# Kernel optimization log

Measured on AMD Instinct MI355X. Metric: run time of the kernel, lower is better.

The kernel has to match this reference:

```python
import jax, jax.numpy as jnp
import numpy as np

N = 50000        # nodes
E = 800000       # edges (before self loops)
F_IN = 128       # input feature dim
HID = 64         # hidden channels per head
HEADS = 4        # heads for layers 1,2 (conv_out has 1 head)
OUT = 40         # num classes
NEG_SLOPE = 0.2  # PyG GATConv default LeakyReLU slope


def gat_layer(x, src, dst, W, att_src, att_dst, b, num_nodes):
    """PyG-style GATConv (concat=True, inference: no dropout).

    x: [N, F_in], W: [F_in, H*C], att_*: [H, C], b: [H*C].
    """
    H, C = att_src.shape
    xw = (x @ W).reshape(num_nodes, H, C)            # [N, H, C]
    a_s = jnp.sum(xw * att_src[None], axis=-1)       # [N, H] per-node src logit
    a_d = jnp.sum(xw * att_dst[None], axis=-1)       # [N, H] per-node dst logit
    e = jax.nn.leaky_relu(a_s[src] + a_d[dst], NEG_SLOPE)  # [E, H]
    # segment softmax over incoming edges of each dst node
    emax = jax.ops.segment_max(e, dst, num_segments=num_nodes)   # [N, H]
    ee = jnp.exp(e - emax[dst])                                  # [E, H]
    denom = jax.ops.segment_sum(ee, dst, num_segments=num_nodes) # [N, H]
    alpha = ee / (denom[dst] + 1e-16)                            # [E, H]
    # scatter-weighted aggregation of source features
    msg = alpha[:, :, None] * xw[src]                            # [E, H, C]
    out = jax.ops.segment_sum(msg, dst, num_segments=num_nodes)  # [N, H, C]
    return out.reshape(num_nodes, H * C) + b


def setup_inputs() -> dict:
    key = jax.random.key(0)
    ks = jax.random.split(key, 12)

    def glorot(k, shape):
        lim = float(np.sqrt(6.0 / (shape[0] + shape[-1])))
        return jax.random.uniform(k, shape, jnp.float32, -lim, lim)

    x = jax.random.normal(ks[0], (N, F_IN), jnp.float32)
    edge_index = jax.random.randint(ks[1], (2, E), 0, N, dtype=jnp.int32)
    inp = {
        "x": x,
        "edge_index": edge_index,
        # layer 1: 128 -> 4 heads x 64
        "W1": glorot(ks[2], (F_IN, HEADS * HID)),
        "a1_src": glorot(ks[3], (HEADS, HID)),
        "a1_dst": glorot(ks[4], (HEADS, HID)),
        "b1": jnp.zeros((HEADS * HID,), jnp.float32),
        # layer 2: 256 -> 4 heads x 64
        "W2": glorot(ks[5], (HEADS * HID, HEADS * HID)),
        "a2_src": glorot(ks[6], (HEADS, HID)),
        "a2_dst": glorot(ks[7], (HEADS, HID)),
        "b2": jnp.zeros((HEADS * HID,), jnp.float32),
        # output layer: 256 -> 1 head x 40
        "W3": glorot(ks[8], (HEADS * HID, OUT)),
        "a3_src": glorot(ks[9], (1, OUT)),
        "a3_dst": glorot(ks[10], (1, OUT)),
        "b3": jnp.zeros((OUT,), jnp.float32),
    }
    return inp


def reference(x, edge_index, W1, a1_src, a1_dst, b1, W2, a2_src, a2_dst, b2,
              W3, a3_src, a3_dst, b3):
    # PyG GATConv adds self loops by default
    loop = jnp.arange(N, dtype=edge_index.dtype)
    src = jnp.concatenate([edge_index[0], loop])
    dst = jnp.concatenate([edge_index[1], loop])

    h = jax.nn.elu(gat_layer(x, src, dst, W1, a1_src, a1_dst, b1, N))
    h = jax.nn.elu(gat_layer(h, src, dst, W2, a2_src, a2_dst, b2, N))
    h = gat_layer(h, src, dst, W3, a3_src, a3_dst, b3, N)
    return jax.nn.log_softmax(h, axis=1)
```

## Files before the change

kernel.cpp:

```cpp
#include <hip/hip_runtime.h>
#include <hip/hip_bf16.h>

#define NN 50000
#define NE 800000

using bf16x8 = __attribute__((ext_vector_type(8))) short;
using f32x4  = __attribute__((ext_vector_type(4))) float;
using f32x2  = __attribute__((ext_vector_type(2))) float;

__device__ __forceinline__ ushort f2bf(float f) {
  uint x = __float_as_uint(f);
  return (ushort)((x + 0x7FFFu + ((x >> 16) & 1u)) >> 16);
}
__device__ __forceinline__ float bf2f(ushort u) {
  return __uint_as_float(((uint)u) << 16);
}
__device__ __forceinline__ float leaky(float x) { return fmaxf(x, 0.2f * x); }

__device__ __forceinline__ unsigned char f32_to_fp8(float v) {
  int pk = __builtin_amdgcn_cvt_pk_fp8_f32(v, v, 0, false);
  return (unsigned char)(pk & 0xff);
}
__device__ __forceinline__ float4 fp8x4_to_f32(uint u) {
  f32x2 lo = __builtin_amdgcn_cvt_pk_f32_fp8((int)u, false);
  f32x2 hi = __builtin_amdgcn_cvt_pk_f32_fp8((int)u, true);
  return make_float4(lo[0], lo[1], hi[0], hi[1]);
}

__device__ __forceinline__ void gload_lds16(const void* g, void* l) {
  __builtin_amdgcn_global_load_lds(
      (const __attribute__((address_space(1))) unsigned int*)g,
      (__attribute__((address_space(3))) unsigned int*)l, 16, 0, 0);
}


__global__ __launch_bounds__(256) void hist_kernel(const int* __restrict__ dst,
                                                   int* __restrict__ counts) {
  int e = blockIdx.x * 256 + threadIdx.x;
  if (e < NE) atomicAdd(&counts[dst[e]], 1);
}

__global__ __launch_bounds__(1024) void scan1_kernel(const int* __restrict__ counts,
                                                     int* __restrict__ partial,
                                                     int* __restrict__ blockSums) {
  __shared__ int sm[1024];
  int i = blockIdx.x * 1024 + threadIdx.x;
  sm[threadIdx.x] = (i < NN) ? counts[i] : 0;
  __syncthreads();
  for (int off = 1; off < 1024; off <<= 1) {
    int t = (threadIdx.x >= off) ? sm[threadIdx.x - off] : 0;
    __syncthreads();
    sm[threadIdx.x] += t;
    __syncthreads();
  }
  if (i < NN) partial[i] = sm[threadIdx.x];
  if (threadIdx.x == 1023) blockSums[blockIdx.x] = sm[1023];
}

__global__ __launch_bounds__(256) void scan23_kernel(const int* __restrict__ partial,
                                                     const int* __restrict__ blockSums,
                                                     int* __restrict__ rowPtr) {
  int i = blockIdx.x * 256 + threadIdx.x;
  if (i < NN) {
    const int nb = i >> 10;
    int off = 0;
    for (int b = 0; b < nb; ++b) off += blockSums[b];
    rowPtr[i + 1] = partial[i] + off;
    if (i == 0) rowPtr[0] = 0;
  }
}

__global__ __launch_bounds__(256) void fill_kernel(const int* __restrict__ srcArr,
                                                   const int* __restrict__ dstArr,
                                                   const int* __restrict__ rowPtr,
                                                   int* __restrict__ cursor,
                                                   int* __restrict__ colSrc) {
  int e = blockIdx.x * 256 + threadIdx.x;
  if (e < NE) {
    int d = dstArr[e];
    int p = rowPtr[d] + atomicAdd(&cursor[d], 1);
    colSrc[p] = srcArr[e];
  }
}


__device__ __forceinline__ void prefrag_one(int idx, const float* __restrict__ W,
                                            const float* __restrict__ atS,
                                            const float* __restrict__ atD,
                                            ushort* __restrict__ Bf,
                                            int Mout, int Mpad, int nh, int Cdim, int KC) {
  const int i = idx & 7;
  const int lane = (idx >> 3) & 63;
  const int kc = (idx >> 9) % KC;
  const int ct = idx / (KC * 512);
  const int k = kc * 32 + (lane >> 4) * 8 + i;
  const int col = ct * 16 + (lane & 15);
  float v = 0.f;
  if (col < Mout) {
    v = W[(size_t)k * Mout + col];
  } else if (col >= Mpad && col < Mpad + nh) {
    const int h = col - Mpad; float s = 0.f;
    for (int c = 0; c < Cdim; ++c) s += W[(size_t)k * Mout + h * Cdim + c] * atS[h * Cdim + c];
    v = s;
  } else if (col >= Mpad + nh && col < Mpad + 2 * nh) {
    const int h = col - Mpad - nh; float s = 0.f;
    for (int c = 0; c < Cdim; ++c) s += W[(size_t)k * Mout + h * Cdim + c] * atD[h * Cdim + c];
    v = s;
  }
  Bf[idx] = f2bf(v);
}

#define T1 (17 * 4 * 512)
#define T2 (17 * 8 * 512)
#define T3 (5 * 8 * 512)

__global__ __launch_bounds__(256) void prefrag_all_kernel(
    const float* __restrict__ W1, const float* __restrict__ a1s, const float* __restrict__ a1d,
    const float* __restrict__ W2, const float* __restrict__ a2s, const float* __restrict__ a2d,
    const float* __restrict__ W3, const float* __restrict__ a3s, const float* __restrict__ a3d,
    ushort* __restrict__ Bf1, ushort* __restrict__ Bf2, ushort* __restrict__ Bf3) {
  int idx = blockIdx.x * 256 + threadIdx.x;
  if (idx < T1) {
    prefrag_one(idx, W1, a1s, a1d, Bf1, 256, 256, 4, 64, 4);
  } else if (idx < T1 + T2) {
    prefrag_one(idx - T1, W2, a2s, a2d, Bf2, 256, 256, 4, 64, 8);
  } else if (idx < T1 + T2 + T3) {
    prefrag_one(idx - T1 - T2, W3, a3s, a3d, Bf3, 40, 64, 1, 40, 8);
  }
}


template <int NCT, int KC, bool AF32, bool OUT8>
__global__ __launch_bounds__(512) void gemm_mfma_kernel(const void* __restrict__ Araw,
                                                        const ushort* __restrict__ Bf,
                                                        void* __restrict__ xwOut,
                                                        float* __restrict__ asB,
                                                        float* __restrict__ adB,
                                                        int Mpad, int nh) {
  __shared__ __align__(16) ushort sB[2][NCT * 512];
  constexpr int K = KC * 32;
  const int lane = threadIdx.x & 63;
  const int w = threadIdx.x >> 6;
  const int rowBase = blockIdx.x * 128 + w * 16;
  const int arow = min(rowBase + (lane & 15), NN - 1);
  const int koff = (lane >> 4) * 8;
  f32x4 acc[NCT];
#pragma unroll
  for (int ct = 0; ct < NCT; ++ct) acc[ct] = (f32x4){0.f, 0.f, 0.f, 0.f};

#pragma unroll
  for (int ct0 = 0; ct0 < NCT; ++ct0) {
    if ((ct0 & 7) == w)
      gload_lds16(Bf + (((size_t)ct0 * KC) << 9) + lane * 8, &sB[0][ct0 * 512]);
  }
  __syncthreads();

#pragma unroll
  for (int kc = 0; kc < KC; ++kc) {
    const int nb = kc & 1;
    if (kc + 1 < KC) {
#pragma unroll
      for (int ct0 = 0; ct0 < NCT; ++ct0) {
        if ((ct0 & 7) == w)
          gload_lds16(Bf + (((size_t)ct0 * KC + kc + 1) << 9) + lane * 8,
                      &sB[nb ^ 1][ct0 * 512]);
      }
    }
    bf16x8 af;
    if constexpr (AF32) {
      const float* ap = (const float*)Araw + (size_t)arow * K + koff + kc * 32;
      float4 p0 = *(const float4*)ap;
      float4 p1 = *(const float4*)(ap + 4);
      af[0] = (short)f2bf(p0.x); af[1] = (short)f2bf(p0.y);
      af[2] = (short)f2bf(p0.z); af[3] = (short)f2bf(p0.w);
      af[4] = (short)f2bf(p1.x); af[5] = (short)f2bf(p1.y);
      af[6] = (short)f2bf(p1.z); af[7] = (short)f2bf(p1.w);
    } else {
      const ushort* ap = (const ushort*)Araw + (size_t)arow * K + koff + kc * 32;
      af = *reinterpret_cast<const bf16x8*>(ap);
    }
#pragma unroll
    for (int ct = 0; ct < NCT; ++ct) {
      bf16x8 bfr = *reinterpret_cast<const bf16x8*>(&sB[nb][ct * 512 + lane * 8]);
      acc[ct] = __builtin_amdgcn_mfma_f32_16x16x32_bf16(af, bfr, acc[ct], 0, 0, 0);
    }
    __syncthreads();
  }

  const int colL = lane & 15;
  const int rquad = (lane >> 4) * 4;
#pragma unroll
  for (int ct = 0; ct < NCT; ++ct) {
    const int col = ct * 16 + colL;
#pragma unroll
    for (int r = 0; r < 4; ++r) {
      const int row = rowBase + rquad + r;
      if (row < NN) {
        const float v = acc[ct][r];
        if (col < Mpad) {
          if constexpr (OUT8) {
            ((unsigned char*)xwOut)[(size_t)row * Mpad + col] = f32_to_fp8(v);
          } else {
            ((ushort*)xwOut)[(size_t)row * Mpad + col] = f2bf(v);
          }
        } else if (col < Mpad + nh) {
          asB[(size_t)row * nh + (col - Mpad)] = v;
        } else if (col < Mpad + 2 * nh) {
          adB[(size_t)row * nh + (col - Mpad - nh)] = v;
        }
      }
    }
  }
}


__global__ __launch_bounds__(256) void aggregate256_kernel(
    const unsigned char* __restrict__ xw, const float* __restrict__ asB,
    const float* __restrict__ adB,
    const int* __restrict__ rowPtr, const int* __restrict__ colSrc,
    const float* __restrict__ bias, ushort* __restrict__ hout, int applyElu) {
  __shared__ int   lsrc[4][64];
  __shared__ float lw[4][256];
  const int n = (blockIdx.x * blockDim.x + threadIdx.x) >> 6;
  if (n >= NN) return;
  const int lane = threadIdx.x & 63;
  const int wv = (threadIdx.x >> 6) & 3;
  const int h = lane >> 4;
  const int ch = lane * 4;
  const int p0 = rowPtr[n], deg = rowPtr[n + 1] - p0;
  const float4 ad4 = *(const float4*)(adB + n * 4);
  const float4 as4 = *(const float4*)(asB + n * 4);
  float4 m;
  m.x = leaky(as4.x + ad4.x); m.y = leaky(as4.y + ad4.y);
  m.z = leaky(as4.z + ad4.z); m.w = leaky(as4.w + ad4.w);
  float4 s = make_float4(1.f, 1.f, 1.f, 1.f);
  float4 acc = fp8x4_to_f32(*(const uint*)(xw + (size_t)n * 256 + ch));

  for (int c0 = 0; c0 < deg; c0 += 64) {
    const int e = c0 + lane;
    const bool valid = e < deg;
    const int src = valid ? colSrc[p0 + e] : n;
    const float4 a4 = *(const float4*)(asB + src * 4);
    float4 ev;
    ev.x = valid ? leaky(a4.x + ad4.x) : -3.0e38f;
    ev.y = valid ? leaky(a4.y + ad4.y) : -3.0e38f;
    ev.z = valid ? leaky(a4.z + ad4.z) : -3.0e38f;
    ev.w = valid ? leaky(a4.w + ad4.w) : -3.0e38f;
    float4 mc = ev;
#pragma unroll
    for (int o = 1; o < 64; o <<= 1) {
      mc.x = fmaxf(mc.x, __shfl_xor(mc.x, o));
      mc.y = fmaxf(mc.y, __shfl_xor(mc.y, o));
      mc.z = fmaxf(mc.z, __shfl_xor(mc.z, o));
      mc.w = fmaxf(mc.w, __shfl_xor(mc.w, o));
    }
    float4 m2;
    m2.x = fmaxf(m.x, mc.x); m2.y = fmaxf(m.y, mc.y);
    m2.z = fmaxf(m.z, mc.z); m2.w = fmaxf(m.w, mc.w);
    float4 sc;
    sc.x = __expf(m.x - m2.x); sc.y = __expf(m.y - m2.y);
    sc.z = __expf(m.z - m2.z); sc.w = __expf(m.w - m2.w);
    const float msc = (h == 0) ? sc.x : (h == 1) ? sc.y : (h == 2) ? sc.z : sc.w;
    acc.x *= msc; acc.y *= msc; acc.z *= msc; acc.w *= msc;
    float4 w4;
    w4.x = valid ? __expf(ev.x - m2.x) : 0.f;
    w4.y = valid ? __expf(ev.y - m2.y) : 0.f;
    w4.z = valid ? __expf(ev.z - m2.z) : 0.f;
    w4.w = valid ? __expf(ev.w - m2.w) : 0.f;
    lsrc[wv][lane] = src;
    *(float4*)&lw[wv][lane * 4] = make_float4(w4.x, w4.y, w4.z, w4.w);
    float4 ss = w4;
#pragma unroll
    for (int o = 1; o < 64; o <<= 1) {
      ss.x += __shfl_xor(ss.x, o);
      ss.y += __shfl_xor(ss.y, o);
      ss.z += __shfl_xor(ss.z, o);
      ss.w += __shfl_xor(ss.w, o);
    }
    s.x = s.x * sc.x + ss.x; s.y = s.y * sc.y + ss.y;
    s.z = s.z * sc.z + ss.z; s.w = s.w * sc.w + ss.w;
    m = m2;
    const int cd = min(64, deg - c0);
    const int cdr = (cd + 7) & ~7;
    for (int j = 0; j < cdr; j += 8) {
      int ssrc[8]; float wj[8];
#pragma unroll
      for (int q = 0; q < 8; ++q) {
        ssrc[q] = lsrc[wv][j + q];
        wj[q] = lw[wv][(j + q) * 4 + h];
      }
      uint u[8];
#pragma unroll
      for (int q = 0; q < 8; ++q)
        u[q] = *(const uint*)(xw + (size_t)ssrc[q] * 256 + ch);
#pragma unroll
      for (int q = 0; q < 8; ++q) {
        const float4 x4 = fp8x4_to_f32(u[q]);
        acc.x += wj[q] * x4.x;
        acc.y += wj[q] * x4.y;
        acc.z += wj[q] * x4.z;
        acc.w += wj[q] * x4.w;
      }
    }
  }

  const float sh = (h == 0) ? s.x : (h == 1) ? s.y : (h == 2) ? s.z : s.w;
  const float inv = 1.f / (sh + 1e-16f);
  const float4 b4 = *(const float4*)(bias + ch);
  float o0 = acc.x * inv + b4.x, o1 = acc.y * inv + b4.y;
  float o2 = acc.z * inv + b4.z, o3 = acc.w * inv + b4.w;
  if (applyElu) {
    o0 = o0 > 0.f ? o0 : __expf(o0) - 1.f;
    o1 = o1 > 0.f ? o1 : __expf(o1) - 1.f;
    o2 = o2 > 0.f ? o2 : __expf(o2) - 1.f;
    o3 = o3 > 0.f ? o3 : __expf(o3) - 1.f;
  }
  ushort4 o4;
  o4.x = f2bf(o0); o4.y = f2bf(o1); o4.z = f2bf(o2); o4.w = f2bf(o3);
  *(ushort4*)(hout + (size_t)n * 256 + ch) = o4;
}


__global__ __launch_bounds__(256) void aggregate40_lsm_kernel(
    const ushort* __restrict__ xw, const float* __restrict__ asB, const float* __restrict__ adB,
    const int* __restrict__ rowPtr, const int* __restrict__ colSrc,
    const float* __restrict__ bias, float* __restrict__ out) {
  __shared__ int   lsrc[4][64];
  __shared__ float lw[4][64];
  const int n = (blockIdx.x * blockDim.x + threadIdx.x) >> 6;
  if (n >= NN) return;
  const int lane = threadIdx.x & 63;
  const int wv = (threadIdx.x >> 6) & 3;
  const bool act = lane < 40;
  const int p0 = rowPtr[n], deg = rowPtr[n + 1] - p0;
  const float adn = adB[n];
  float m = leaky(asB[n] + adn);
  float s = 1.f;
  float acc = bf2f(xw[(size_t)n * 64 + lane]);

  for (int c0 = 0; c0 < deg; c0 += 64) {
    const int e = c0 + lane;
    const bool valid = e < deg;
    const int src = valid ? colSrc[p0 + e] : n;
    const float a = asB[src];
    float ev = valid ? leaky(a + adn) : -3.0e38f;
    float mc = ev;
#pragma unroll
    for (int o = 1; o < 64; o <<= 1) mc = fmaxf(mc, __shfl_xor(mc, o));
    const float m2 = fmaxf(m, mc);
    const float scl = __expf(m - m2);
    acc *= scl;
    float wv_ = valid ? __expf(ev - m2) : 0.f;
    lsrc[wv][lane] = src;
    lw[wv][lane] = wv_;
    float ss = wv_;
#pragma unroll
    for (int o = 1; o < 64; o <<= 1) ss += __shfl_xor(ss, o);
    s = s * scl + ss;
    m = m2;
    const int cd = min(64, deg - c0);
    const int cdr = (cd + 7) & ~7;
    for (int j = 0; j < cdr; j += 8) {
      int ssrc[8]; float wj[8];
#pragma unroll
      for (int q = 0; q < 8; ++q) { ssrc[q] = lsrc[wv][j + q]; wj[q] = lw[wv][j + q]; }
      ushort u[8];
#pragma unroll
      for (int q = 0; q < 8; ++q) u[q] = xw[(size_t)ssrc[q] * 64 + lane];
#pragma unroll
      for (int q = 0; q < 8; ++q) acc += wj[q] * bf2f(u[q]);
    }
  }

  float val = acc / (s + 1e-16f) + (act ? bias[lane] : 0.f);
  float v = act ? val : -1e30f;
  float mx = v;
#pragma unroll
  for (int o = 1; o < 64; o <<= 1) mx = fmaxf(mx, __shfl_xor(mx, o));
  float ex = act ? __expf(val - mx) : 0.f;
#pragma unroll
  for (int o = 1; o < 64; o <<= 1) ex += __shfl_xor(ex, o);
  if (act) out[(size_t)n * 40 + lane] = val - mx - __logf(ex);
}


extern "C" void kernel_launch(void* const* d_in, const int* in_sizes, int n_in,
                              void* d_out, int out_size, void* d_ws, size_t ws_size,
                              hipStream_t stream) {
  const float* x   = (const float*)d_in[0];
  const int*   ei  = (const int*)d_in[1];
  const float* W1  = (const float*)d_in[2];
  const float* a1s = (const float*)d_in[3];
  const float* a1d = (const float*)d_in[4];
  const float* b1  = (const float*)d_in[5];
  const float* W2  = (const float*)d_in[6];
  const float* a2s = (const float*)d_in[7];
  const float* a2d = (const float*)d_in[8];
  const float* b2  = (const float*)d_in[9];
  const float* W3  = (const float*)d_in[10];
  const float* a3s = (const float*)d_in[11];
  const float* a3d = (const float*)d_in[12];
  const float* b3  = (const float*)d_in[13];
  float* out = (float*)d_out;

  char* w = (char*)d_ws;
  unsigned char* xwBuf = (unsigned char*)w;  w += (size_t)NN * 256;
  ushort* hBuf  = (ushort*)w;  w += (size_t)NN * 256 * 2;
  ushort* xw40  = (ushort*)w;  w += (size_t)NN * 64 * 2;
  float* asBuf  = (float*)w;   w += (size_t)NN * 4 * 4;
  float* adBuf  = (float*)w;   w += (size_t)NN * 4 * 4;
  ushort* Bf1   = (ushort*)w;  w += (size_t)T1 * 2;
  ushort* Bf2   = (ushort*)w;  w += (size_t)T2 * 2;
  ushort* Bf3   = (ushort*)w;  w += (size_t)T3 * 2;
  int* counts   = (int*)w;     w += (size_t)NN * 4;
  int* cursor   = (int*)w;     w += (size_t)NN * 4;
  int* rowPtr   = (int*)w;     w += (size_t)(NN + 1) * 4;
  int* colSrc   = (int*)w;     w += (size_t)NE * 4;
  int* partial  = (int*)w;     w += (size_t)NN * 4;
  int* blockSums = (int*)w;    w += 64 * 4;

  const int nScanBlocks = (NN + 1023) / 1024;

  hipMemsetAsync(counts, 0, (size_t)2 * NN * 4, stream);
  hist_kernel<<<(NE + 255) / 256, 256, 0, stream>>>(ei + NE, counts);
  scan1_kernel<<<nScanBlocks, 1024, 0, stream>>>(counts, partial, blockSums);
  scan23_kernel<<<(NN + 255) / 256, 256, 0, stream>>>(partial, blockSums, rowPtr);
  fill_kernel<<<(NE + 255) / 256, 256, 0, stream>>>(ei, ei + NE, rowPtr, cursor, colSrc);

  prefrag_all_kernel<<<(T1 + T2 + T3 + 255) / 256, 256, 0, stream>>>(
      W1, a1s, a1d, W2, a2s, a2d, W3, a3s, a3d, Bf1, Bf2, Bf3);

  const int gemmBlocks = (NN + 127) / 128;
  const int nodeBlocks = NN / 4;

  gemm_mfma_kernel<17, 4, true, true><<<gemmBlocks, 512, 0, stream>>>(x, Bf1, xwBuf, asBuf, adBuf, 256, 4);
  aggregate256_kernel<<<nodeBlocks, 256, 0, stream>>>(xwBuf, asBuf, adBuf, rowPtr, colSrc, b1, hBuf, 1);

  gemm_mfma_kernel<17, 8, false, true><<<gemmBlocks, 512, 0, stream>>>(hBuf, Bf2, xwBuf, asBuf, adBuf, 256, 4);
  aggregate256_kernel<<<nodeBlocks, 256, 0, stream>>>(xwBuf, asBuf, adBuf, rowPtr, colSrc, b2, hBuf, 1);

  gemm_mfma_kernel<5, 8, false, false><<<gemmBlocks, 512, 0, stream>>>(hBuf, Bf3, xw40, asBuf, adBuf, 64, 1);
  aggregate40_lsm_kernel<<<nodeBlocks, 256, 0, stream>>>(xw40, asBuf, adBuf, rowPtr, colSrc, b3, out);
}
```

Baseline: 389.3 us.

## Register-block GEMM over two row tiles and add single-pass low-degree aggregation

The GEMM now runs 4 waves per block, and each wave computes two 16-row tiles that share every B fragment read from LDS. This halves LDS B traffic per MFMA but doubles accumulator registers, which can lower occupancy for NCT=17. The aggregation kernels add a fast path for nodes with degree at most 64. That path does one-pass softmax without online rescaling, pre-shifts the source indices into byte offsets, and unrolls the gather by 4 instead of 8, trading fewer rescale ops for less memory-level parallelism per iteration.

```diff
diff --git a/kernel.cpp b/kernel.cpp
--- a/kernel.cpp
+++ b/kernel.cpp
@@ -131,7 +131,7 @@
 
 
 template <int NCT, int KC, bool AF32, bool OUT8>
-__global__ __launch_bounds__(512) void gemm_mfma_kernel(const void* __restrict__ Araw,
+__global__ __launch_bounds__(256) void gemm_mfma_kernel(const void* __restrict__ Araw,
                                                         const ushort* __restrict__ Bf,
                                                         void* __restrict__ xwOut,
                                                         float* __restrict__ asB,
@@ -141,16 +141,21 @@
   constexpr int K = KC * 32;
   const int lane = threadIdx.x & 63;
   const int w = threadIdx.x >> 6;
-  const int rowBase = blockIdx.x * 128 + w * 16;
-  const int arow = min(rowBase + (lane & 15), NN - 1);
+  const int rowBase0 = blockIdx.x * 128 + w * 16;
+  const int rowBase1 = rowBase0 + 64;
+  const int arow0 = min(rowBase0 + (lane & 15), NN - 1);
+  const int arow1 = min(rowBase1 + (lane & 15), NN - 1);
   const int koff = (lane >> 4) * 8;
-  f32x4 acc[NCT];
-#pragma unroll
-  for (int ct = 0; ct < NCT; ++ct) acc[ct] = (f32x4){0.f, 0.f, 0.f, 0.f};
+  f32x4 acc0[NCT], acc1[NCT];
+#pragma unroll
+  for (int ct = 0; ct < NCT; ++ct) {
+    acc0[ct] = (f32x4){0.f, 0.f, 0.f, 0.f};
+    acc1[ct] = (f32x4){0.f, 0.f, 0.f, 0.f};
+  }
 
 #pragma unroll
   for (int ct0 = 0; ct0 < NCT; ++ct0) {
-    if ((ct0 & 7) == w)
+    if ((ct0 & 3) == w)
       gload_lds16(Bf + (((size_t)ct0 * KC) << 9) + lane * 8, &sB[0][ct0 * 512]);
   }
   __syncthreads();
@@ -161,28 +166,36 @@
     if (kc + 1 < KC) {
 #pragma unroll
       for (int ct0 = 0; ct0 < NCT; ++ct0) {
-        if ((ct0 & 7) == w)
+        if ((ct0 & 3) == w)
           gload_lds16(Bf + (((size_t)ct0 * KC + kc + 1) << 9) + lane * 8,
                       &sB[nb ^ 1][ct0 * 512]);
       }
     }
-    bf16x8 af;
+    bf16x8 af0, af1;
     if constexpr (AF32) {
-      const float* ap = (const float*)Araw + (size_t)arow * K + koff + kc * 32;
-      float4 p0 = *(const float4*)ap;
-      float4 p1 = *(const float4*)(ap + 4);
-      af[0] = (short)f2bf(p0.x); af[1] = (short)f2bf(p0.y);
-      af[2] = (short)f2bf(p0.z); af[3] = (short)f2bf(p0.w);
-      af[4] = (short)f2bf(p1.x); af[5] = (short)f2bf(p1.y);
-      af[6] = (short)f2bf(p1.z); af[7] = (short)f2bf(p1.w);
+      const float* ap0 = (const float*)Araw + (size_t)arow0 * K + koff + kc * 32;
+      const float* ap1 = (const float*)Araw + (size_t)arow1 * K + koff + kc * 32;
+      float4 p0 = *(const float4*)ap0, p1 = *(const float4*)(ap0 + 4);
+      float4 q0 = *(const float4*)ap1, q1 = *(const float4*)(ap1 + 4);
+      af0[0] = (short)f2bf(p0.x); af0[1] = (short)f2bf(p0.y);
+      af0[2] = (short)f2bf(p0.z); af0[3] = (short)f2bf(p0.w);
+      af0[4] = (short)f2bf(p1.x); af0[5] = (short)f2bf(p1.y);
+      af0[6] = (short)f2bf(p1.z); af0[7] = (short)f2bf(p1.w);
+      af1[0] = (short)f2bf(q0.x); af1[1] = (short)f2bf(q0.y);
+      af1[2] = (short)f2bf(q0.z); af1[3] = (short)f2bf(q0.w);
+      af1[4] = (short)f2bf(q1.x); af1[5] = (short)f2bf(q1.y);
+      af1[6] = (short)f2bf(q1.z); af1[7] = (short)f2bf(q1.w);
     } else {
-      const ushort* ap = (const ushort*)Araw + (size_t)arow * K + koff + kc * 32;
-      af = *reinterpret_cast<const bf16x8*>(ap);
+      const ushort* ap0 = (const ushort*)Araw + (size_t)arow0 * K + koff + kc * 32;
+      const ushort* ap1 = (const ushort*)Araw + (size_t)arow1 * K + koff + kc * 32;
+      af0 = *reinterpret_cast<const bf16x8*>(ap0);
+      af1 = *reinterpret_cast<const bf16x8*>(ap1);
     }
 #pragma unroll
     for (int ct = 0; ct < NCT; ++ct) {
       bf16x8 bfr = *reinterpret_cast<const bf16x8*>(&sB[nb][ct * 512 + lane * 8]);
-      acc[ct] = __builtin_amdgcn_mfma_f32_16x16x32_bf16(af, bfr, acc[ct], 0, 0, 0);
+      acc0[ct] = __builtin_amdgcn_mfma_f32_16x16x32_bf16(af0, bfr, acc0[ct], 0, 0, 0);
+      acc1[ct] = __builtin_amdgcn_mfma_f32_16x16x32_bf16(af1, bfr, acc1[ct], 0, 0, 0);
     }
     __syncthreads();
   }
@@ -190,23 +203,27 @@
   const int colL = lane & 15;
   const int rquad = (lane >> 4) * 4;
 #pragma unroll
-  for (int ct = 0; ct < NCT; ++ct) {
-    const int col = ct * 16 + colL;
-#pragma unroll
-    for (int r = 0; r < 4; ++r) {
-      const int row = rowBase + rquad + r;
-      if (row < NN) {
-        const float v = acc[ct][r];
-        if (col < Mpad) {
-          if constexpr (OUT8) {
-            ((unsigned char*)xwOut)[(size_t)row * Mpad + col] = f32_to_fp8(v);
-          } else {
-            ((ushort*)xwOut)[(size_t)row * Mpad + col] = f2bf(v);
+  for (int half = 0; half < 2; ++half) {
+    const int rb = half ? rowBase1 : rowBase0;
+#pragma unroll
+    for (int ct = 0; ct < NCT; ++ct) {
+      const int col = ct * 16 + colL;
+#pragma unroll
+      for (int r = 0; r < 4; ++r) {
+        const int row = rb + rquad + r;
+        if (row < NN) {
+          const float v = half ? acc1[ct][r] : acc0[ct][r];
+          if (col < Mpad) {
+            if constexpr (OUT8) {
+              ((unsigned char*)xwOut)[(size_t)row * Mpad + col] = f32_to_fp8(v);
+            } else {
+              ((ushort*)xwOut)[(size_t)row * Mpad + col] = f2bf(v);
+            }
+          } else if (col < Mpad + nh) {
+            asB[(size_t)row * nh + (col - Mpad)] = v;
+          } else if (col < Mpad + 2 * nh) {
+            adB[(size_t)row * nh + (col - Mpad - nh)] = v;
           }
-        } else if (col < Mpad + nh) {
-          asB[(size_t)row * nh + (col - Mpad)] = v;
-        } else if (col < Mpad + 2 * nh) {
-          adB[(size_t)row * nh + (col - Mpad - nh)] = v;
         }
       }
     }
@@ -230,16 +247,15 @@
   const int p0 = rowPtr[n], deg = rowPtr[n + 1] - p0;
   const float4 ad4 = *(const float4*)(adB + n * 4);
   const float4 as4 = *(const float4*)(asB + n * 4);
+  float4 es;
+  es.x = leaky(as4.x + ad4.x); es.y = leaky(as4.y + ad4.y);
+  es.z = leaky(as4.z + ad4.z); es.w = leaky(as4.w + ad4.w);
+  float4 s, acc;
   float4 m;
-  m.x = leaky(as4.x + ad4.x); m.y = leaky(as4.y + ad4.y);
-  m.z = leaky(as4.z + ad4.z); m.w = leaky(as4.w + ad4.w);
-  float4 s = make_float4(1.f, 1.f, 1.f, 1.f);
-  float4 acc = fp8x4_to_f32(*(const uint*)(xw + (size_t)n * 256 + ch));
-
-  for (int c0 = 0; c0 < deg; c0 += 64) {
-    const int e = c0 + lane;
-    const bool valid = e < deg;
-    const int src = valid ? colSrc[p0 + e] : n;
+
+  if (deg <= 64) {
+    const bool valid = lane < deg;
+    const int src = valid ? colSrc[p0 + lane] : n;
     const float4 a4 = *(const float4*)(asB + src * 4);
     float4 ev;
     ev.x = valid ? leaky(a4.x + ad4.x) : -3.0e38f;
@@ -254,21 +270,15 @@
       mc.z = fmaxf(mc.z, __shfl_xor(mc.z, o));
       mc.w = fmaxf(mc.w, __shfl_xor(mc.w, o));
     }
-    float4 m2;
-    m2.x = fmaxf(m.x, mc.x); m2.y = fmaxf(m.y, mc.y);
-    m2.z = fmaxf(m.z, mc.z); m2.w = fmaxf(m.w, mc.w);
-    float4 sc;
-    sc.x = __expf(m.x - m2.x); sc.y = __expf(m.y - m2.y);
-    sc.z = __expf(m.z - m2.z); sc.w = __expf(m.w - m2.w);
-    const float msc = (h == 0) ? sc.x : (h == 1) ? sc.y : (h == 2) ? sc.z : sc.w;
-    acc.x *= msc; acc.y *= msc; acc.z *= msc; acc.w *= msc;
+    m.x = fmaxf(es.x, mc.x); m.y = fmaxf(es.y, mc.y);
+    m.z = fmaxf(es.z, mc.z); m.w = fmaxf(es.w, mc.w);
     float4 w4;
-    w4.x = valid ? __expf(ev.x - m2.x) : 0.f;
-    w4.y = valid ? __expf(ev.y - m2.y) : 0.f;
-    w4.z = valid ? __expf(ev.z - m2.z) : 0.f;
-    w4.w = valid ? __expf(ev.w - m2.w) : 0.f;
-    lsrc[wv][lane] = src;
-    *(float4*)&lw[wv][lane * 4] = make_float4(w4.x, w4.y, w4.z, w4.w);
+    w4.x = valid ? __expf(ev.x - m.x) : 0.f;
+    w4.y = valid ? __expf(ev.y - m.y) : 0.f;
+    w4.z = valid ? __expf(ev.z - m.z) : 0.f;
+    w4.w = valid ? __expf(ev.w - m.w) : 0.f;
+    lsrc[wv][lane] = src << 8;
+    *(float4*)&lw[wv][lane * 4] = w4;
     float4 ss = w4;
 #pragma unroll
     for (int o = 1; o < 64; o <<= 1) {
@@ -277,29 +287,101 @@
       ss.z += __shfl_xor(ss.z, o);
       ss.w += __shfl_xor(ss.w, o);
     }
-    s.x = s.x * sc.x + ss.x; s.y = s.y * sc.y + ss.y;
-    s.z = s.z * sc.z + ss.z; s.w = s.w * sc.w + ss.w;
-    m = m2;
-    const int cd = min(64, deg - c0);
-    const int cdr = (cd + 7) & ~7;
-    for (int j = 0; j < cdr; j += 8) {
-      int ssrc[8]; float wj[8];
-#pragma unroll
-      for (int q = 0; q < 8; ++q) {
-        ssrc[q] = lsrc[wv][j + q];
-        wj[q] = lw[wv][(j + q) * 4 + h];
+    float4 wself;
+    wself.x = __expf(es.x - m.x); wself.y = __expf(es.y - m.y);
+    wself.z = __expf(es.z - m.z); wself.w = __expf(es.w - m.w);
+    s.x = wself.x + ss.x; s.y = wself.y + ss.y;
+    s.z = wself.z + ss.z; s.w = wself.w + ss.w;
+    const float wsh = (h == 0) ? wself.x : (h == 1) ? wself.y : (h == 2) ? wself.z : wself.w;
+    const float4 x4 = fp8x4_to_f32(*(const uint*)(xw + (size_t)n * 256 + ch));
+    acc = make_float4(wsh * x4.x, wsh * x4.y, wsh * x4.z, wsh * x4.w);
+    const int cdr = (deg + 3) & ~3;
+    for (int j = 0; j < cdr; j += 4) {
+      const int o0 = lsrc[wv][j + 0], o1 = lsrc[wv][j + 1];
+      const int o2 = lsrc[wv][j + 2], o3 = lsrc[wv][j + 3];
+      const float w0 = lw[wv][(j + 0) * 4 + h];
+      const float w1 = lw[wv][(j + 1) * 4 + h];
+      const float w2 = lw[wv][(j + 2) * 4 + h];
+      const float w3 = lw[wv][(j + 3) * 4 + h];
+      const uint u0 = *(const uint*)(xw + o0 + ch);
+      const uint u1 = *(const uint*)(xw + o1 + ch);
+      const uint u2 = *(const uint*)(xw + o2 + ch);
+      const uint u3 = *(const uint*)(xw + o3 + ch);
+      const float4 x0 = fp8x4_to_f32(u0), x1 = fp8x4_to_f32(u1);
+      const float4 x2 = fp8x4_to_f32(u2), x3 = fp8x4_to_f32(u3);
+      acc.x += w0 * x0.x + w1 * x1.x + w2 * x2.x + w3 * x3.x;
+      acc.y += w0 * x0.y + w1 * x1.y + w2 * x2.y + w3 * x3.y;
+      acc.z += w0 * x0.z + w1 * x1.z + w2 * x2.z + w3 * x3.z;
+      acc.w += w0 * x0.w + w1 * x1.w + w2 * x2.w + w3 * x3.w;
+    }
+  } else {
+    m = es;
+    s = make_float4(1.f, 1.f, 1.f, 1.f);
+    const float4 x4 = fp8x4_to_f32(*(const uint*)(xw + (size_t)n * 256 + ch));
+    acc = make_float4(x4.x, x4.y, x4.z, x4.w);
+    for (int c0 = 0; c0 < deg; c0 += 64) {
+      const int e = c0 + lane;
+      const bool valid = e < deg;
+      const int src = valid ? colSrc[p0 + e] : n;
+      const float4 a4 = *(const float4*)(asB + src * 4);
+      float4 ev;
+      ev.x = valid ? leaky(a4.x + ad4.x) : -3.0e38f;
+      ev.y = valid ? leaky(a4.y + ad4.y) : -3.0e38f;
+      ev.z = valid ? leaky(a4.z + ad4.z) : -3.0e38f;
+      ev.w = valid ? leaky(a4.w + ad4.w) : -3.0e38f;
+      float4 mc = ev;
+#pragma unroll
+      for (int o = 1; o < 64; o <<= 1) {
+        mc.x = fmaxf(mc.x, __shfl_xor(mc.x, o));
+        mc.y = fmaxf(mc.y, __shfl_xor(mc.y, o));
+        mc.z = fmaxf(mc.z, __shfl_xor(mc.z, o));
+        mc.w = fmaxf(mc.w, __shfl_xor(mc.w, o));
       }
-      uint u[8];
-#pragma unroll
-      for (int q = 0; q < 8; ++q)
-        u[q] = *(const uint*)(xw + (size_t)ssrc[q] * 256 + ch);
-#pragma unroll
-      for (int q = 0; q < 8; ++q) {
-        const float4 x4 = fp8x4_to_f32(u[q]);
-        acc.x += wj[q] * x4.x;
-        acc.y += wj[q] * x4.y;
-        acc.z += wj[q] * x4.z;
-        acc.w += wj[q] * x4.w;
+      float4 m2;
+      m2.x = fmaxf(m.x, mc.x); m2.y = fmaxf(m.y, mc.y);
+      m2.z = fmaxf(m.z, mc.z); m2.w = fmaxf(m.w, mc.w);
+      float4 sc;
+      sc.x = __expf(m.x - m2.x); sc.y = __expf(m.y - m2.y);
+      sc.z = __expf(m.z - m2.z); sc.w = __expf(m.w - m2.w);
+      const float msc = (h == 0) ? sc.x : (h == 1) ? sc.y : (h == 2) ? sc.z : sc.w;
+      acc.x *= msc; acc.y *= msc; acc.z *= msc; acc.w *= msc;
+      float4 w4;
+      w4.x = valid ? __expf(ev.x - m2.x) : 0.f;
+      w4.y = valid ? __expf(ev.y - m2.y) : 0.f;
+      w4.z = valid ? __expf(ev.z - m2.z) : 0.f;
+      w4.w = valid ? __expf(ev.w - m2.w) : 0.f;
+      lsrc[wv][lane] = src << 8;
+      *(float4*)&lw[wv][lane * 4] = w4;
+      float4 ss = w4;
+#pragma unroll
+      for (int o = 1; o < 64; o <<= 1) {
+        ss.x += __shfl_xor(ss.x, o);
+        ss.y += __shfl_xor(ss.y, o);
+        ss.z += __shfl_xor(ss.z, o);
+        ss.w += __shfl_xor(ss.w, o);
+      }
+      s.x = s.x * sc.x + ss.x; s.y = s.y * sc.y + ss.y;
+      s.z = s.z * sc.z + ss.z; s.w = s.w * sc.w + ss.w;
+      m = m2;
+      const int cd = min(64, deg - c0);
+      const int cdr = (cd + 3) & ~3;
+      for (int j = 0; j < cdr; j += 4) {
+        const int o0 = lsrc[wv][j + 0], o1 = lsrc[wv][j + 1];
+        const int o2 = lsrc[wv][j + 2], o3 = lsrc[wv][j + 3];
+        const float w0 = lw[wv][(j + 0) * 4 + h];
+        const float w1 = lw[wv][(j + 1) * 4 + h];
+        const float w2 = lw[wv][(j + 2) * 4 + h];
+        const float w3 = lw[wv][(j + 3) * 4 + h];
+        const uint u0 = *(const uint*)(xw + o0 + ch);
+        const uint u1 = *(const uint*)(xw + o1 + ch);
+        const uint u2 = *(const uint*)(xw + o2 + ch);
+        const uint u3 = *(const uint*)(xw + o3 + ch);
+        const float4 x0 = fp8x4_to_f32(u0), x1 = fp8x4_to_f32(u1);
+        const float4 x2 = fp8x4_to_f32(u2), x3 = fp8x4_to_f32(u3);
+        acc.x += w0 * x0.x + w1 * x1.x + w2 * x2.x + w3 * x3.x;
+        acc.y += w0 * x0.y + w1 * x1.y + w2 * x2.y + w3 * x3.y;
+        acc.z += w0 * x0.z + w1 * x1.z + w2 * x2.z + w3 * x3.z;
+        acc.w += w0 * x0.w + w1 * x1.w + w2 * x2.w + w3 * x3.w;
       }
     }
   }
@@ -334,41 +416,70 @@
   const bool act = lane < 40;
   const int p0 = rowPtr[n], deg = rowPtr[n + 1] - p0;
   const float adn = adB[n];
-  float m = leaky(asB[n] + adn);
-  float s = 1.f;
-  float acc = bf2f(xw[(size_t)n * 64 + lane]);
-
-  for (int c0 = 0; c0 < deg; c0 += 64) {
-    const int e = c0 + lane;
-    const bool valid = e < deg;
-    const int src = valid ? colSrc[p0 + e] : n;
-    const float a = asB[src];
-    float ev = valid ? leaky(a + adn) : -3.0e38f;
+  const float es = leaky(asB[n] + adn);
+  float m, s, acc;
+
+  if (deg <= 64) {
+    const bool valid = lane < deg;
+    const int src = valid ? colSrc[p0 + lane] : n;
+    float ev = valid ? leaky(asB[src] + adn) : -3.0e38f;
     float mc = ev;
 #pragma unroll
     for (int o = 1; o < 64; o <<= 1) mc = fmaxf(mc, __shfl_xor(mc, o));
-    const float m2 = fmaxf(m, mc);
-    const float scl = __expf(m - m2);
-    acc *= scl;
-    float wv_ = valid ? __expf(ev - m2) : 0.f;
-    lsrc[wv][lane] = src;
+    m = fmaxf(es, mc);
+    const float wv_ = valid ? __expf(ev - m) : 0.f;
+    lsrc[wv][lane] = src << 6;
     lw[wv][lane] = wv_;
     float ss = wv_;
 #pragma unroll
     for (int o = 1; o < 64; o <<= 1) ss += __shfl_xor(ss, o);
-    s = s * scl + ss;
-    m = m2;
-    const int cd = min(64, deg - c0);
-    const int cdr = (cd + 7) & ~7;
-    for (int j = 0; j < cdr; j += 8) {
-      int ssrc[8]; float wj[8];
-#pragma unroll
-      for (int q = 0; q < 8; ++q) { ssrc[q] = lsrc[wv][j + q]; wj[q] = lw[wv][j + q]; }
-      ushort u[8];
-#pragma unroll
-      for (int q = 0; q < 8; ++q) u[q] = xw[(size_t)ssrc[q] * 64 + lane];
-#pragma unroll
-      for (int q = 0; q < 8; ++q) acc += wj[q] * bf2f(u[q]);
+    const float wself = __expf(es - m);
+    s = wself + ss;
+    acc = wself * bf2f(xw[(size_t)n * 64 + lane]);
+    const int cdr = (deg + 3) & ~3;
+    for (int j = 0; j < cdr; j += 4) {
+      const int o0 = lsrc[wv][j + 0], o1 = lsrc[wv][j + 1];
+      const int o2 = lsrc[wv][j + 2], o3 = lsrc[wv][j + 3];
+      const float w0 = lw[wv][j + 0], w1 = lw[wv][j + 1];
+      const float w2 = lw[wv][j + 2], w3 = lw[wv][j + 3];
+      const float x0 = bf2f(xw[o0 + lane]);
+      const float x1 = bf2f(xw[o1 + lane]);
+      const float x2 = bf2f(xw[o2 + lane]);
+      const float x3 = bf2f(xw[o3 + lane]);
+      acc += w0 * x0 + w1 * x1 + w2 * x2 + w3 * x3;
+    }
+  } else {
+    m = es; s = 1.f;
+    acc = bf2f(xw[(size_t)n * 64 + lane]);
+    for (int c0 = 0; c0 < deg; c0 += 64) {
+      const int e = c0 + lane;
+      const bool valid = e < deg;
+      const int src = valid ? colSrc[p0 + e] : n;
+      float ev = valid ? leaky(asB[src] + adn) : -3.0e38f;
+      float mc = ev;
+#pragma unroll
+      for (int o = 1; o < 64; o <<= 1) mc = fmaxf(mc, __shfl_xor(mc, o));
+      const float m2 = fmaxf(m, mc);
+      const float scl = __expf(m - m2);
+      acc *= scl;
+      float wv_ = valid ? __expf(ev - m2) : 0.f;
+      lsrc[wv][lane] = src << 6;
+      lw[wv][lane] = wv_;
+      float ss = wv_;
+#pragma unroll
+      for (int o = 1; o < 64; o <<= 1) ss += __shfl_xor(ss, o);
+      s = s * scl + ss;
+      m = m2;
+      const int cd = min(64, deg - c0);
+      const int cdr = (cd + 3) & ~3;
+      for (int j = 0; j < cdr; j += 4) {
+        const int o0 = lsrc[wv][j + 0], o1 = lsrc[wv][j + 1];
+        const int o2 = lsrc[wv][j + 2], o3 = lsrc[wv][j + 3];
+        const float w0 = lw[wv][j + 0], w1 = lw[wv][j + 1];
+        const float w2 = lw[wv][j + 2], w3 = lw[wv][j + 3];
+        acc += w0 * bf2f(xw[o0 + lane]) + w1 * bf2f(xw[o1 + lane]) +
+               w2 * bf2f(xw[o2 + lane]) + w3 * bf2f(xw[o3 + lane]);
+      }
     }
   }
 
@@ -433,12 +544,12 @@
   const int gemmBlocks = (NN + 127) / 128;
   const int nodeBlocks = NN / 4;
 
-  gemm_mfma_kernel<17, 4, true, true><<<gemmBlocks, 512, 0, stream>>>(x, Bf1, xwBuf, asBuf, adBuf, 256, 4);
+  gemm_mfma_kernel<17, 4, true, true><<<gemmBlocks, 256, 0, stream>>>(x, Bf1, xwBuf, asBuf, adBuf, 256, 4);
   aggregate256_kernel<<<nodeBlocks, 256, 0, stream>>>(xwBuf, asBuf, adBuf, rowPtr, colSrc, b1, hBuf, 1);
 
-  gemm_mfma_kernel<17, 8, false, true><<<gemmBlocks, 512, 0, stream>>>(hBuf, Bf2, xwBuf, asBuf, adBuf, 256, 4);
+  gemm_mfma_kernel<17, 8, false, true><<<gemmBlocks, 256, 0, stream>>>(hBuf, Bf2, xwBuf, asBuf, adBuf, 256, 4);
   aggregate256_kernel<<<nodeBlocks, 256, 0, stream>>>(xwBuf, asBuf, adBuf, rowPtr, colSrc, b2, hBuf, 1);
 
-  gemm_mfma_kernel<5, 8, false, false><<<gemmBlocks, 512, 0, stream>>>(hBuf, Bf3, xw40, asBuf, adBuf, 64, 1);
+  gemm_mfma_kernel<5, 8, false, false><<<gemmBlocks, 256, 0, stream>>>(hBuf, Bf3, xw40, asBuf, adBuf, 64, 1);
   aggregate40_lsm_kernel<<<nodeBlocks, 256, 0, stream>>>(xw40, asBuf, adBuf, rowPtr, colSrc, b3, out);
 }
```

New measurement: 389.3 us. No clear change (+0.0%).
